# Optimization experiments

Hardware: AMD Instinct MI355X
Metric: run time of the kernel (lower is better)

## Reference

```python
import jax, jax.numpy as jnp
import numpy as np

B, N, D, L, NREPEAT = 32, 577, 384, 12, 4
H = 4 * D  # mlp hidden
EPS = 1e-6


def ln(x, w, b):
    mu = jnp.mean(x, axis=-1, keepdims=True)
    var = jnp.mean(jnp.square(x - mu), axis=-1, keepdims=True)
    return (x - mu) * jax.lax.rsqrt(var + EPS) * w + b


def setup_inputs() -> dict:
    key = jax.random.key(0)
    ks = jax.random.split(key, 16)
    s = 0.02
    return {
        "x": jax.random.normal(ks[0], (B, N, D), dtype=jnp.float32),
        "norm1_w": jnp.ones((L, D), jnp.float32),
        "norm1_b": jnp.zeros((L, D), jnp.float32),
        "qkv_w": jax.random.normal(ks[1], (L, 3 * D, D), jnp.float32) * s,
        "qkv_b": jnp.zeros((L, 3 * D), jnp.float32),
        "qn_w": jnp.ones((L, D), jnp.float32),
        "qn_b": jnp.zeros((L, D), jnp.float32),
        "kn_w": jnp.ones((L, D), jnp.float32),
        "kn_b": jnp.zeros((L, D), jnp.float32),
        "an_w": jnp.ones((L, D), jnp.float32),
        "an_b": jnp.zeros((L, D), jnp.float32),
        "proj_w": jax.random.normal(ks[2], (L, D, D), jnp.float32) * s,
        "proj_b": jnp.zeros((L, D), jnp.float32),
        "ls1": jnp.full((L, D), 1e-5, jnp.float32),
        "norm2_w": jnp.ones((L, D), jnp.float32),
        "norm2_b": jnp.zeros((L, D), jnp.float32),
        "fc1_w": jax.random.normal(ks[3], (L, H, D), jnp.float32) * s,
        "fc1_b": jnp.zeros((L, H), jnp.float32),
        "fc2_w": jax.random.normal(ks[4], (L, D, H), jnp.float32) * s,
        "fc2_b": jnp.zeros((L, D), jnp.float32),
        "ls2": jnp.full((L, D), 1e-5, jnp.float32),
    }


def _forward(x, norm1_w, norm1_b, qkv_w, qkv_b, qn_w, qn_b, kn_w, kn_b,
             an_w, an_b, proj_w, proj_b, ls1, norm2_w, norm2_b,
             fc1_w, fc1_b, fc2_w, fc2_b, ls2):
    scale = 1.0 / np.sqrt(D).astype(np.float32)
    x_prime = x
    history = []  # list of [B, 1, D] cls tokens, grows each repeat
    for _ in range(NREPEAT):
        new_cls = x[:, 0:1]
        x = jnp.concatenate([new_cls, x_prime[:, 1:]], axis=1)  # [B, N, D]
        mem = jnp.concatenate([x] + history, axis=1)            # [B, N+t, D]
        for l in range(L):
            res1 = x
            xn = ln(x, norm1_w[l], norm1_b[l])
            # manual qkv split: q from normed x, k/v from UNNORMED mem
            q = xn @ qkv_w[l, :D].T + qkv_b[l, :D]
            k = mem @ qkv_w[l, D:2 * D].T + qkv_b[l, D:2 * D]
            v = mem @ qkv_w[l, 2 * D:].T + qkv_b[l, 2 * D:]
            q = ln(q, qn_w[l], qn_b[l])
            k = ln(k, kn_w[l], kn_b[l])
            # single-head SDPA over full width D
            attn = jax.nn.softmax(jnp.einsum('bqd,bkd->bqk', q, k) * scale, axis=-1)
            prod = jnp.einsum('bqk,bkd->bqd', attn, v)
            prod = ln(prod, an_w[l], an_b[l])
            proj = prod @ proj_w[l].T + proj_b[l]
            x = proj * ls1[l] + res1
            res2 = x
            x2 = ln(x, norm2_w[l], norm2_b[l])
            h = jax.nn.gelu(x2 @ fc1_w[l].T + fc1_b[l], approximate=False)
            x1 = h @ fc2_w[l].T + fc2_b[l]
            x = x1 * ls2[l] + res2
        history.append(new_cls)
    return x


def reference(x, norm1_w, norm1_b, qkv_w, qkv_b, qn_w, qn_b, kn_w, kn_b,
              an_w, an_b, proj_w, proj_b, ls1, norm2_w, norm2_b,
              fc1_w, fc1_b, fc2_w, fc2_b, ls2):
    return _forward(x, norm1_w, norm1_b, qkv_w, qkv_b, qn_w, qn_b, kn_w, kn_b,
                    an_w, an_b, proj_w, proj_b, ls1, norm2_w, norm2_b,
                    fc1_w, fc1_b, fc2_w, fc2_b, ls2)
```

## Files before the change

kernel.cpp:

```cpp
#include <hip/hip_runtime.h>
#include <math.h>

#define BB 32
#define NN 577
#define DD 384
#define HD 1536
#define LL 12
#define MP 640
#define NRPT 4

typedef __attribute__((ext_vector_type(8))) short bf16x8;
typedef __attribute__((ext_vector_type(4))) float f32x4;

__device__ __forceinline__ unsigned short f2bf(float f){
  unsigned u = __builtin_bit_cast(unsigned, f);
  u += 0x7fffu + ((u >> 16) & 1u);
  return (unsigned short)(u >> 16);
}
__device__ __forceinline__ float bf2f(unsigned short s){
  unsigned u = ((unsigned)s) << 16;
  return __builtin_bit_cast(float, u);
}

__device__ __forceinline__ void async16(void* lds, const void* g){
  __builtin_amdgcn_global_load_lds(
      (const __attribute__((address_space(1))) unsigned int*)g,
      (__attribute__((address_space(3))) unsigned int*)lds, 16, 0, 0);
}

__global__ void prep_k(float* __restrict__ x, const float* __restrict__ xp,
                       float* __restrict__ cls_r, const float* __restrict__ cls_hist,
                       unsigned short* __restrict__ mem, int r){
  int i = blockIdx.x * 256 + threadIdx.x;
  if (i >= BB*MP*DD) return;
  int d = i % DD;
  int n = (i / DD) % MP;
  int b = i / (MP*DD);
  float v;
  if (n == 0){ v = x[(size_t)b*NN*DD + d]; cls_r[b*DD + d] = v; }
  else if (n < NN){ v = xp[((size_t)b*NN + n)*DD + d]; x[((size_t)b*NN + n)*DD + d] = v; }
  else if (n < NN + r){ v = cls_hist[(size_t)(n-NN)*BB*DD + b*DD + d]; }
  else v = 0.f;
  mem[i] = f2bf(v);
}

__global__ void castL_k(const float* __restrict__ qkvw, const float* __restrict__ pw,
                        const float* __restrict__ f1w, const float* __restrict__ f2w,
                        unsigned short* __restrict__ wbuf){
  int i = blockIdx.x * 256 + threadIdx.x;
  const int QKV = 3*DD*DD;
  const int PRJ = DD*DD;
  const int F1  = HD*DD;
  const int TOT = QKV + PRJ + 2*F1;
  if (i >= TOT) return;
  float v;
  if (i < QKV) v = qkvw[i];
  else if (i < QKV+PRJ) v = pw[i-QKV];
  else if (i < QKV+PRJ+F1) v = f1w[i-QKV-PRJ];
  else v = f2w[i-QKV-PRJ-F1];
  wbuf[i] = f2bf(v);
}

template<typename T>
__global__ __launch_bounds__(256) void ln4_k(const T* __restrict__ in, const float* __restrict__ w,
                                             const float* __restrict__ bias, unsigned short* __restrict__ out,
                                             int nrows){
  int row = blockIdx.x*4 + (threadIdx.x >> 6);
  if (row >= nrows) return;
  int lane = threadIdx.x & 63;
  const T* p = in + (size_t)row*DD;
  float v[6];
  float s = 0.f;
  #pragma unroll
  for (int i=0;i<6;i++){
    float t;
    if (sizeof(T) == 4) t = (float)p[lane + i*64];
    else t = bf2f((unsigned short)p[lane + i*64]);
    v[i] = t; s += t;
  }
  #pragma unroll
  for (int o=32;o;o>>=1) s += __shfl_xor(s, o, 64);
  float mu = s * (1.f/DD);
  float q = 0.f;
  #pragma unroll
  for (int i=0;i<6;i++){ float t = v[i]-mu; q += t*t; }
  #pragma unroll
  for (int o=32;o;o>>=1) q += __shfl_xor(q, o, 64);
  float rs = rsqrtf(q*(1.f/DD) + 1e-6f);
  unsigned short* po = out + (size_t)row*DD;
  #pragma unroll
  for (int i=0;i<6;i++){
    int c = lane + i*64;
    po[c] = f2bf((v[i]-mu)*rs*w[c] + bias[c]);
  }
}


template<int EPI>
__global__ __launch_bounds__(256) void gemm128(
    const unsigned short* __restrict__ A, int lda, int arows, long sA,
    const unsigned short* __restrict__ B, int ldb, int brows, long sB,
    const float* __restrict__ bias,
    int K, int N,
    float* __restrict__ outF, unsigned short* __restrict__ outB,
    int ldo, int orows, long sO,
    const float* __restrict__ ls){

  __shared__ unsigned short a_sh[2][128*32];
  __shared__ unsigned short b_sh[2][128*32];

  int tid  = threadIdx.x;
  int wave = tid >> 6, lane = tid & 63;
  int lr = lane & 15, kg = lane >> 4;
  int wm = wave >> 1, wn = wave & 1;
  int z = blockIdx.z;
  int row0 = blockIdx.y * 128;
  int col0 = blockIdx.x * 128;

  const unsigned short* Ab = A + (size_t)z*sA;
  const unsigned short* Bb = B + (size_t)z*sB;

  f32x4 zf = {0.f,0.f,0.f,0.f};
  f32x4 acc[4][4];
  #pragma unroll
  for (int i=0;i<4;i++)
    #pragma unroll
    for (int j=0;j<4;j++) acc[i][j] = zf;

  int ra[2], rb[2], kc[2];
  #pragma unroll
  for (int it=0; it<2; it++){
    int c = tid + it*256;
    int r = row0 + (c>>2); if (r > arows-1) r = arows-1;
    ra[it] = r;
    r = col0 + (c>>2); if (r > brows-1) r = brows-1;
    rb[it] = r;
    kc[it] = (c&3)*8;
  }

  for (int k0 = 0; k0 < K; k0 += 64){
    #pragma unroll
    for (int p=0;p<2;p++){
      #pragma unroll
      for (int it=0; it<2; it++){
        unsigned short* la = &a_sh[p][(it*256 + wave*64)*8];
        unsigned short* lb = &b_sh[p][(it*256 + wave*64)*8];
        async16(la, Ab + (size_t)ra[it]*lda + k0 + p*32 + kc[it]);
        async16(lb, Bb + (size_t)rb[it]*ldb + k0 + p*32 + kc[it]);
      }
    }
    __syncthreads();
    #pragma unroll
    for (int p=0;p<2;p++){
      bf16x8 af[4], bfr[4];
      #pragma unroll
      for (int i=0;i<4;i++){
        af[i]  = *(const bf16x8*)&a_sh[p][(wm*64 + i*16 + lr)*32 + kg*8];
        bfr[i] = *(const bf16x8*)&b_sh[p][(wn*64 + i*16 + lr)*32 + kg*8];
      }
      #pragma unroll
      for (int i=0;i<4;i++)
        #pragma unroll
        for (int j=0;j<4;j++)
          acc[i][j] = __builtin_amdgcn_mfma_f32_16x16x32_bf16(af[i], bfr[j], acc[i][j], 0,0,0);
    }
    __syncthreads();
  }

  float* oF = outF ? outF + (size_t)z*sO : nullptr;
  unsigned short* oB = outB ? outB + (size_t)z*sO : nullptr;

  #pragma unroll
  for (int mi=0;mi<4;mi++)
    #pragma unroll
    for (int ni=0;ni<4;ni++)
      #pragma unroll
      for (int r=0;r<4;r++){
        int row = row0 + wm*64 + mi*16 + kg*4 + r;
        int col = col0 + wn*64 + ni*16 + lr;
        if (row >= orows || col >= N) continue;
        float vv = acc[mi][ni][r];
        size_t idx = (size_t)row*ldo + col;
        if (EPI == 0){
          if (bias) vv += bias[col];
          oB[idx] = f2bf(vv);
        } else if (EPI == 1){
          vv += bias[row];
          oB[idx] = f2bf(vv);
        } else if (EPI == 2){
          vv += bias[col];
          oF[idx] = vv*ls[col] + oF[idx];
        } else {
          vv += bias[col];
          float g = 0.5f*vv*(1.f + erff(vv*0.70710678118f));
          oB[idx] = f2bf(g);
        }
      }
}

__global__ __launch_bounds__(256) void softmax4_k(const unsigned short* __restrict__ S,
                                                  unsigned short* __restrict__ P, int M){
  int row = blockIdx.x*4 + (threadIdx.x >> 6);
  int m = row % MP;
  int lane = threadIdx.x & 63;
  unsigned short* po = P + (size_t)row*MP;
  if (m >= NN){
    for (int n = lane; n < MP; n += 64) po[n] = 0;
    return;
  }
  const unsigned short* ps = S + (size_t)row*MP;
  const float scale = 0.05103103588f;
  float t[10];
  float mx = -INFINITY;
  #pragma unroll
  for (int i=0;i<10;i++){
    int n = lane + i*64;
    float v = (n < M) ? bf2f(ps[n])*scale : -INFINITY;
    t[i] = v; mx = fmaxf(mx, v);
  }
  #pragma unroll
  for (int o=32;o;o>>=1) mx = fmaxf(mx, __shfl_xor(mx, o, 64));
  float s = 0.f;
  #pragma unroll
  for (int i=0;i<10;i++){
    int n = lane + i*64;
    float e = (n < M) ? expf(t[i]-mx) : 0.f;
    t[i] = e; s += e;
  }
  #pragma unroll
  for (int o=32;o;o>>=1) s += __shfl_xor(s, o, 64);
  float inv = 1.f / s;
  #pragma unroll
  for (int i=0;i<10;i++){
    int n = lane + i*64;
    po[n] = f2bf(t[i]*inv);
  }
}


extern "C" void kernel_launch(void* const* d_in, const int* in_sizes, int n_in,
                              void* d_out, int out_size, void* d_ws, size_t ws_size,
                              hipStream_t stream){
  const float* x_in = (const float*)d_in[0];
  const float* n1w  = (const float*)d_in[1];
  const float* n1b  = (const float*)d_in[2];
  const float* qkvw = (const float*)d_in[3];
  const float* qkvb = (const float*)d_in[4];
  const float* qnw  = (const float*)d_in[5];
  const float* qnb  = (const float*)d_in[6];
  const float* knw  = (const float*)d_in[7];
  const float* knb  = (const float*)d_in[8];
  const float* anw  = (const float*)d_in[9];
  const float* anb  = (const float*)d_in[10];
  const float* pw   = (const float*)d_in[11];
  const float* pb   = (const float*)d_in[12];
  const float* ls1  = (const float*)d_in[13];
  const float* n2w  = (const float*)d_in[14];
  const float* n2b  = (const float*)d_in[15];
  const float* f1w  = (const float*)d_in[16];
  const float* f1b  = (const float*)d_in[17];
  const float* f2w  = (const float*)d_in[18];
  const float* f2bb = (const float*)d_in[19];
  const float* ls2  = (const float*)d_in[20];

  char* ws = (char*)d_ws;
  size_t off = 0;
  auto alloc = [&](size_t bytes)->char* {
    char* p = ws + off;
    off = (off + bytes + 255) & ~(size_t)255;
    return p;
  };

  const int QKV = 3*DD*DD, PRJ = DD*DD, F1 = HD*DD;
  const size_t WTOT = (size_t)QKV + PRJ + 2*F1;
  const size_t SLOT = (size_t)BB*MP*DD;

  unsigned short* wbuf  = (unsigned short*)alloc(WTOT*2);
  float*          cls_h = (float*)         alloc((size_t)NRPT*BB*DD*4);
  unsigned short* mem_bf= (unsigned short*)alloc(SLOT*2);
  unsigned short* pool  = (unsigned short*)alloc(6*SLOT*2);

  unsigned short* wq = wbuf;
  unsigned short* wp = wbuf + QKV;
  unsigned short* w1 = wbuf + QKV + PRJ;
  unsigned short* w2 = wbuf + QKV + PRJ + F1;

  unsigned short* S0 = pool;
  unsigned short* S1 = pool + SLOT;
  unsigned short* S2 = pool + 2*SLOT;
  unsigned short* S3 = pool + 3*SLOT;
  unsigned short* S4 = pool + 4*SLOT;
  unsigned short* S5 = pool + 5*SLOT;

  unsigned short* xn    = S0;
  unsigned short* qraw  = S1;
  unsigned short* kraw  = S2;
  unsigned short* qb    = S3;
  unsigned short* kb    = S4;
  unsigned short* vT    = S5;
  unsigned short* Ssc   = S1;
  unsigned short* Pbf   = S3;
  unsigned short* prod  = S0;
  unsigned short* prodn = S1;
  unsigned short* x2    = S0;
  unsigned short* h     = S1;

  float* xf = (float*)d_out;

  auto cg = [](size_t n){ return dim3((unsigned)((n + 255) / 256)); };

  hipMemcpyAsync(xf, x_in, (size_t)BB*NN*DD*4, hipMemcpyDeviceToDevice, stream);

  const int RT   = (BB*NN + 127)/128;
  const int RTM  = (BB*MP)/128;
  const int QR   = BB*NN;
  const int KR   = BB*MP;

  for (int r = 0; r < NRPT; r++){
    int M = NN + r;
    prep_k<<<cg((size_t)BB*MP*DD),256,0,stream>>>(xf, x_in, cls_h + (size_t)r*BB*DD, cls_h, mem_bf, r);
    for (int l = 0; l < LL; l++){
      castL_k<<<cg(WTOT),256,0,stream>>>(qkvw + (size_t)l*QKV, pw + (size_t)l*PRJ,
                                         f1w + (size_t)l*F1, f2w + (size_t)l*F1, wbuf);
      ln4_k<float><<<cg((size_t)QR*64),256,0,stream>>>(xf, n1w + l*DD, n1b + l*DD, xn, QR);
      gemm128<0><<<dim3(3,RT,1),256,0,stream>>>(xn,384,QR,0, wq,384,384,0,
          qkvb + l*3*DD, 384,384, nullptr,qraw,384,QR,0, nullptr);
      gemm128<0><<<dim3(3,RTM,1),256,0,stream>>>(mem_bf,384,KR,0, wq + (size_t)DD*DD,384,384,0,
          qkvb + l*3*DD + DD, 384,384, nullptr,kraw,384,KR,0, nullptr);
      gemm128<1><<<dim3(MP/128,3,BB),256,0,stream>>>(wq + (size_t)2*DD*DD,384,384,0, mem_bf,384,MP,(long)MP*DD,
          qkvb + l*3*DD + 2*DD, 384,MP, nullptr,vT,MP,384,(long)DD*MP, nullptr);
      ln4_k<unsigned short><<<cg((size_t)QR*64),256,0,stream>>>(qraw, qnw + l*DD, qnb + l*DD, qb, QR);
      ln4_k<unsigned short><<<cg((size_t)KR*64),256,0,stream>>>(kraw, knw + l*DD, knb + l*DD, kb, KR);
      gemm128<0><<<dim3(MP/128,MP/128,BB),256,0,stream>>>(qb,384,NN,(long)NN*DD, kb,384,MP,(long)MP*DD,
          nullptr, 384,MP, nullptr,Ssc,MP,NN,(long)MP*MP, nullptr);
      softmax4_k<<<KR/4,256,0,stream>>>(Ssc, Pbf, M);
      gemm128<0><<<dim3(3,MP/128,BB),256,0,stream>>>(Pbf,MP,MP,(long)MP*MP, vT,MP,DD,(long)DD*MP,
          nullptr, MP,DD, nullptr,prod,DD,NN,(long)NN*DD, nullptr);
      ln4_k<unsigned short><<<cg((size_t)QR*64),256,0,stream>>>(prod, anw + l*DD, anb + l*DD, prodn, QR);
      gemm128<2><<<dim3(3,RT,1),256,0,stream>>>(prodn,384,QR,0, wp,384,384,0,
          pb + l*DD, 384,384, xf,nullptr,384,QR,0, ls1 + l*DD);
      ln4_k<float><<<cg((size_t)QR*64),256,0,stream>>>(xf, n2w + l*DD, n2b + l*DD, x2, QR);
      gemm128<3><<<dim3(HD/128,RT,1),256,0,stream>>>(x2,384,QR,0, w1,384,HD,0,
          f1b + l*HD, 384,HD, nullptr,h,HD,QR,0, nullptr);
      gemm128<2><<<dim3(3,RT,1),256,0,stream>>>(h,HD,QR,0, w2,HD,384,0,
          f2bb + l*DD, HD,384, xf,nullptr,384,QR,0, ls2 + l*DD);
    }
  }
}
```

Baseline: 17.30 ms.

## Fuse QK-norm launches and replace attention GEMMs with flash-style attention kernel

Merges the separate q and k LayerNorm launches into one kernel that also folds the softmax scale into q. Replaces the score GEMM, the softmax kernel, the PV GEMM and the output LayerNorm with a single online-softmax attention kernel. It keeps q fragments in registers, streams K and V^T tiles through swizzled LDS, and applies the output LayerNorm in the epilogue. This removes the materialised 640x640 score and probability matrices and several launches. In exchange it adds heavy register pressure (24 accumulator tiles), the grid is only 320 blocks, and the LayerNorm variance is computed as E[x^2]-mu^2.

```diff
diff --git a/kernel.cpp b/kernel.cpp
--- a/kernel.cpp
+++ b/kernel.cpp
@@ -95,6 +95,39 @@
   }
 }
 
+__global__ __launch_bounds__(256) void lnqk_k(const unsigned short* __restrict__ qraw,
+                                              const unsigned short* __restrict__ kraw,
+                                              const float* __restrict__ qw, const float* __restrict__ qbias,
+                                              const float* __restrict__ kw, const float* __restrict__ kbias,
+                                              unsigned short* __restrict__ qo, unsigned short* __restrict__ ko){
+  const int QR = BB*NN;
+  int row = blockIdx.x*4 + (threadIdx.x >> 6);
+  int lane = threadIdx.x & 63;
+  bool isq = row < QR;
+  const unsigned short* p = isq ? qraw + (size_t)row*DD : kraw + (size_t)(row-QR)*DD;
+  const float* w  = isq ? qw : kw;
+  const float* bs = isq ? qbias : kbias;
+  unsigned short* po = isq ? qo + (size_t)row*DD : ko + (size_t)(row-QR)*DD;
+  float scale = isq ? 0.05103103588f : 1.0f;
+  float v[6];
+  float s = 0.f;
+  #pragma unroll
+  for (int i=0;i<6;i++){ float t = bf2f(p[lane + i*64]); v[i] = t; s += t; }
+  #pragma unroll
+  for (int o=32;o;o>>=1) s += __shfl_xor(s, o, 64);
+  float mu = s * (1.f/DD);
+  float q = 0.f;
+  #pragma unroll
+  for (int i=0;i<6;i++){ float t = v[i]-mu; q += t*t; }
+  #pragma unroll
+  for (int o=32;o;o>>=1) q += __shfl_xor(q, o, 64);
+  float rs = rsqrtf(q*(1.f/DD) + 1e-6f);
+  #pragma unroll
+  for (int i=0;i<6;i++){
+    int c = lane + i*64;
+    po[c] = f2bf(((v[i]-mu)*rs*w[c] + bs[c]) * scale);
+  }
+}
 
 template<int EPI>
 __global__ __launch_bounds__(256) void gemm128(
@@ -198,42 +231,154 @@
       }
 }
 
-__global__ __launch_bounds__(256) void softmax4_k(const unsigned short* __restrict__ S,
-                                                  unsigned short* __restrict__ P, int M){
-  int row = blockIdx.x*4 + (threadIdx.x >> 6);
-  int m = row % MP;
-  int lane = threadIdx.x & 63;
-  unsigned short* po = P + (size_t)row*MP;
-  if (m >= NN){
-    for (int n = lane; n < MP; n += 64) po[n] = 0;
-    return;
-  }
-  const unsigned short* ps = S + (size_t)row*MP;
-  const float scale = 0.05103103588f;
-  float t[10];
-  float mx = -INFINITY;
-  #pragma unroll
-  for (int i=0;i<10;i++){
-    int n = lane + i*64;
-    float v = (n < M) ? bf2f(ps[n])*scale : -INFINITY;
-    t[i] = v; mx = fmaxf(mx, v);
-  }
-  #pragma unroll
-  for (int o=32;o;o>>=1) mx = fmaxf(mx, __shfl_xor(mx, o, 64));
-  float s = 0.f;
-  #pragma unroll
-  for (int i=0;i<10;i++){
-    int n = lane + i*64;
-    float e = (n < M) ? expf(t[i]-mx) : 0.f;
-    t[i] = e; s += e;
-  }
-  #pragma unroll
-  for (int o=32;o;o>>=1) s += __shfl_xor(s, o, 64);
-  float inv = 1.f / s;
-  #pragma unroll
-  for (int i=0;i<10;i++){
-    int n = lane + i*64;
-    po[n] = f2bf(t[i]*inv);
+__global__ __launch_bounds__(256, 2) void attn_k(
+    const unsigned short* __restrict__ qs,
+    const unsigned short* __restrict__ kb,
+    const unsigned short* __restrict__ vT,
+    const float* __restrict__ anw, const float* __restrict__ anb,
+    unsigned short* __restrict__ out, int M){
+
+  __shared__ unsigned short k_sh[32*384];
+  __shared__ unsigned short v_sh[384*32];
+  __shared__ unsigned short p_sh[64*56];
+
+  int tid = threadIdx.x;
+  int wv = tid >> 6, lane = tid & 63;
+  int lr = lane & 15, kg = lane >> 4;
+  int b = blockIdx.y, qt0 = blockIdx.x * 64;
+
+  bf16x8 qf[12];
+  {
+    int qrow = qt0 + wv*16 + lr; if (qrow > NN-1) qrow = NN-1;
+    const unsigned short* qp = qs + ((size_t)b*NN + qrow)*DD;
+    #pragma unroll
+    for (int ks=0; ks<12; ks++) qf[ks] = *(const bf16x8*)(qp + ks*32 + kg*8);
+  }
+
+  f32x4 zf = {0.f,0.f,0.f,0.f};
+  f32x4 O[24];
+  #pragma unroll
+  for (int i=0;i<24;i++) O[i] = zf;
+  float m_run[4], l_run[4];
+  #pragma unroll
+  for (int r=0;r<4;r++){ m_run[r] = -INFINITY; l_run[r] = 0.f; }
+
+  for (int kt=0; kt<19; kt++){
+    __syncthreads();
+    #pragma unroll
+    for (int i=0;i<6;i++){
+      int L = i*256 + tid;
+      int row = L/48, c = L%48;
+      int gc = (c & ~7) | ((c ^ row) & 7);
+      async16(&k_sh[L*8], kb + ((size_t)b*MP + kt*32 + row)*DD + gc*8);
+    }
+    #pragma unroll
+    for (int i=0;i<6;i++){
+      int L = i*256 + tid;
+      int row = L>>2;
+      int gc = (L&3) ^ (row&3);
+      async16(&v_sh[L*8], vT + ((size_t)b*DD + row)*MP + kt*32 + gc*8);
+    }
+    __syncthreads();
+
+    f32x4 s[2] = {zf, zf};
+    #pragma unroll
+    for (int ks=0; ks<12; ks++){
+      int c = ks*4 + kg;
+      #pragma unroll
+      for (int nk=0; nk<2; nk++){
+        int krow = nk*16 + lr;
+        bf16x8 bk = *(const bf16x8*)&k_sh[krow*DD + ((c & ~7) | ((c ^ krow)&7))*8];
+        s[nk] = __builtin_amdgcn_mfma_f32_16x16x32_bf16(qf[ks], bk, s[nk], 0,0,0);
+      }
+    }
+    #pragma unroll
+    for (int nk=0; nk<2; nk++){
+      if (kt*32 + nk*16 + lr >= M){
+        s[nk][0] = -INFINITY; s[nk][1] = -INFINITY; s[nk][2] = -INFINITY; s[nk][3] = -INFINITY;
+      }
+    }
+    float al[4];
+    #pragma unroll
+    for (int r=0;r<4;r++){
+      float v = fmaxf(s[0][r], s[1][r]);
+      v = fmaxf(v, __shfl_xor(v, 1, 64));
+      v = fmaxf(v, __shfl_xor(v, 2, 64));
+      v = fmaxf(v, __shfl_xor(v, 4, 64));
+      v = fmaxf(v, __shfl_xor(v, 8, 64));
+      float mn = fmaxf(m_run[r], v);
+      al[r] = __expf(m_run[r] - mn);
+      m_run[r] = mn;
+    }
+    #pragma unroll
+    for (int nk=0;nk<2;nk++)
+      #pragma unroll
+      for (int r=0;r<4;r++)
+        s[nk][r] = __expf(s[nk][r] - m_run[r]);
+    #pragma unroll
+    for (int r=0;r<4;r++){
+      float v = s[0][r] + s[1][r];
+      v += __shfl_xor(v, 1, 64);
+      v += __shfl_xor(v, 2, 64);
+      v += __shfl_xor(v, 4, 64);
+      v += __shfl_xor(v, 8, 64);
+      l_run[r] = al[r]*l_run[r] + v;
+    }
+    #pragma unroll
+    for (int nk=0;nk<2;nk++)
+      #pragma unroll
+      for (int r=0;r<4;r++)
+        p_sh[(wv*16 + kg*4 + r)*56 + nk*16 + lr] = f2bf(s[nk][r]);
+    #pragma unroll
+    for (int ni=0;ni<24;ni++)
+      #pragma unroll
+      for (int r=0;r<4;r++) O[ni][r] *= al[r];
+    __syncthreads();
+
+    bf16x8 ap = *(const bf16x8*)&p_sh[(wv*16 + lr)*56 + kg*8];
+    #pragma unroll
+    for (int ni=0;ni<24;ni++){
+      int d = ni*16 + lr;
+      bf16x8 bv = *(const bf16x8*)&v_sh[d*32 + ((kg ^ (d&3))*8)];
+      O[ni] = __builtin_amdgcn_mfma_f32_16x16x32_bf16(ap, bv, O[ni], 0,0,0);
+    }
+  }
+
+  float inv[4];
+  #pragma unroll
+  for (int r=0;r<4;r++) inv[r] = 1.f / l_run[r];
+  float s1[4] = {0,0,0,0}, s2[4] = {0,0,0,0};
+  #pragma unroll
+  for (int ni=0;ni<24;ni++)
+    #pragma unroll
+    for (int r=0;r<4;r++){
+      float x = O[ni][r]*inv[r];
+      O[ni][r] = x;
+      s1[r] += x; s2[r] += x*x;
+    }
+  #pragma unroll
+  for (int r=0;r<4;r++){
+    #pragma unroll
+    for (int o=1;o<16;o<<=1){ s1[r] += __shfl_xor(s1[r], o, 64); s2[r] += __shfl_xor(s2[r], o, 64); }
+  }
+  float mu[4], rs[4];
+  #pragma unroll
+  for (int r=0;r<4;r++){
+    mu[r] = s1[r]*(1.f/DD);
+    float var = s2[r]*(1.f/DD) - mu[r]*mu[r];
+    rs[r] = rsqrtf(fmaxf(var, 0.f) + 1e-6f);
+  }
+  int rowb = qt0 + wv*16 + kg*4;
+  #pragma unroll
+  for (int ni=0;ni<24;ni++){
+    int col = ni*16 + lr;
+    float wc = anw[col], bc = anb[col];
+    #pragma unroll
+    for (int r=0;r<4;r++){
+      int qrow = rowb + r;
+      if (qrow < NN)
+        out[((size_t)b*NN + qrow)*DD + col] = f2bf((O[ni][r]-mu[r])*rs[r]*wc + bc);
+    }
   }
 }
 
@@ -298,9 +443,6 @@
   unsigned short* qb    = S3;
   unsigned short* kb    = S4;
   unsigned short* vT    = S5;
-  unsigned short* Ssc   = S1;
-  unsigned short* Pbf   = S3;
-  unsigned short* prod  = S0;
   unsigned short* prodn = S1;
   unsigned short* x2    = S0;
   unsigned short* h     = S1;
@@ -311,10 +453,10 @@
 
   hipMemcpyAsync(xf, x_in, (size_t)BB*NN*DD*4, hipMemcpyDeviceToDevice, stream);
 
-  const int RT   = (BB*NN + 127)/128;
-  const int RTM  = (BB*MP)/128;
-  const int QR   = BB*NN;
-  const int KR   = BB*MP;
+  const int RT  = (BB*NN + 127)/128;
+  const int RTM = (BB*MP)/128;
+  const int QR  = BB*NN;
+  const int KR  = BB*MP;
 
   for (int r = 0; r < NRPT; r++){
     int M = NN + r;
@@ -329,14 +471,9 @@
           qkvb + l*3*DD + DD, 384,384, nullptr,kraw,384,KR,0, nullptr);
       gemm128<1><<<dim3(MP/128,3,BB),256,0,stream>>>(wq + (size_t)2*DD*DD,384,384,0, mem_bf,384,MP,(long)MP*DD,
           qkvb + l*3*DD + 2*DD, 384,MP, nullptr,vT,MP,384,(long)DD*MP, nullptr);
-      ln4_k<unsigned short><<<cg((size_t)QR*64),256,0,stream>>>(qraw, qnw + l*DD, qnb + l*DD, qb, QR);
-      ln4_k<unsigned short><<<cg((size_t)KR*64),256,0,stream>>>(kraw, knw + l*DD, knb + l*DD, kb, KR);
-      gemm128<0><<<dim3(MP/128,MP/128,BB),256,0,stream>>>(qb,384,NN,(long)NN*DD, kb,384,MP,(long)MP*DD,
-          nullptr, 384,MP, nullptr,Ssc,MP,NN,(long)MP*MP, nullptr);
-      softmax4_k<<<KR/4,256,0,stream>>>(Ssc, Pbf, M);
-      gemm128<0><<<dim3(3,MP/128,BB),256,0,stream>>>(Pbf,MP,MP,(long)MP*MP, vT,MP,DD,(long)DD*MP,
-          nullptr, MP,DD, nullptr,prod,DD,NN,(long)NN*DD, nullptr);
-      ln4_k<unsigned short><<<cg((size_t)QR*64),256,0,stream>>>(prod, anw + l*DD, anb + l*DD, prodn, QR);
+      lnqk_k<<<(QR+KR)/4,256,0,stream>>>(qraw, kraw, qnw + l*DD, qnb + l*DD,
+                                         knw + l*DD, knb + l*DD, qb, kb);
+      attn_k<<<dim3(10,BB),256,0,stream>>>(qb, kb, vT, anw + l*DD, anb + l*DD, prodn, M);
       gemm128<2><<<dim3(3,RT,1),256,0,stream>>>(prodn,384,QR,0, wp,384,384,0,
           pb + l*DD, 384,384, xf,nullptr,384,QR,0, ls1 + l*DD);
       ln4_k<float><<<cg((size_t)QR*64),256,0,stream>>>(xf, n2w + l*DD, n2b + l*DD, x2, QR);
```

After: 16.88 ms. 2.4% less time.
